# Kernel tuning notes

Measured on AMD Instinct MI355X. Metric: run time of the kernel, lower is better.

The kernel has to match this reference:

```python
import jax, jax.numpy as jnp
import numpy as np

CODEBOOK_DIM = 64
CODEBOOK_SLOTS = 512
TEMPERATURE = 0.5
BS, H, W = 16, 64, 64
EPS_G = 1e-10  # gumbel numerical floor
EPS_P = 1e-9   # matches probs.add(1e-09) in torch code


def setup_inputs() -> dict:
    key = jax.random.key(0)
    k1, k2, k3 = jax.random.split(key, 3)
    ze = jax.random.normal(k1, (BS, CODEBOOK_DIM, H, W), dtype=jnp.float32)
    codebook = jax.random.normal(k2, (CODEBOOK_SLOTS, CODEBOOK_DIM), dtype=jnp.float32)
    # uniform noise for Gumbel reparameterization of RelaxedOneHotCategorical.rsample
    u = jax.random.uniform(k3, (BS * H * W, CODEBOOK_SLOTS), dtype=jnp.float32)
    return {"ze": ze, "codebook": codebook, "u": u}


def reference(ze, codebook, u):
    bs, d, h, w = ze.shape
    K = codebook.shape[0]
    log_K = jnp.log(jnp.float32(K))
    # [bs, d, h, w] -> [N, d]
    ze_flat = jnp.transpose(ze, (0, 2, 3, 1)).reshape(-1, d)
    # squared euclidean distances via addmm: ||c||^2 + ||z||^2 - 2 z c^T  -> [N, K]
    distances = (
        jnp.sum(codebook * codebook, axis=1)[None, :]
        + jnp.sum(ze_flat * ze_flat, axis=1, keepdims=True)
        - 2.0 * (ze_flat @ codebook.T)
    )
    logits = -distances
    # Gumbel-softmax (relaxed one-hot categorical rsample)
    gumbel = -jnp.log(-jnp.log(u + EPS_G) + EPS_G)
    soft_onehot = jax.nn.softmax((logits + gumbel) / TEMPERATURE, axis=1)
    hard_indices = jnp.argmax(soft_onehot, axis=1).reshape(bs, h, w)
    # weighted codebook lookup: [N, K] @ [K, d] -> [bs, h, w, d] -> [bs, d, h, w]
    z_q = jnp.transpose((soft_onehot @ codebook).reshape(bs, h, w, d), (0, 3, 1, 2))
    probs = jax.nn.softmax(logits, axis=1)
    KL = jnp.mean(jnp.sum((probs * (jnp.log(probs + EPS_P) + log_K)).reshape(bs, -1), axis=1))
    commit_loss = jnp.mean(jnp.sum((probs * distances).reshape(bs, -1), axis=1))
    return (z_q, hard_indices, KL, commit_loss)
```

## Files before the change

kernel.cpp:

```cpp
#include <hip/hip_runtime.h>
#include <math.h>
#include <stdint.h>

#define IDX_OFF 4194304
#define KL_OFF  4259840
#define CM_OFF  4259841
#define LOG_K   6.238324625039508f

typedef _Float16 half8 __attribute__((ext_vector_type(8)));
typedef _Float16 half4 __attribute__((ext_vector_type(4)));
typedef float f32x4 __attribute__((ext_vector_type(4)));

__device__ __forceinline__ float sh16sum(float v){
#pragma unroll
  for (int m = 1; m < 16; m <<= 1) v += __shfl_xor(v, m, 64);
  return v;
}
__device__ __forceinline__ float sh16max(float v){
#pragma unroll
  for (int m = 1; m < 16; m <<= 1) v = fmaxf(v, __shfl_xor(v, m, 64));
  return v;
}

__global__ __launch_bounds__(64) void vq_pack(const float* __restrict__ cbk, void* __restrict__ ws){
  _Float16* W1H = (_Float16*)ws;
  _Float16* W1L = W1H + 32768;
  _Float16* W2H = W1L + 32768;
  float*    CCw = (float*)(W2H + 32768);
  const int slot = blockIdx.x, c = threadIdx.x;
  const float x = cbk[(slot << 6) + c];
  const _Float16 h = (_Float16)x;
  W1H[(slot << 6) + c] = h;
  W1L[(slot << 6) + c] = (_Float16)(x - (float)h);
  W2H[(c << 9) + slot] = h;
  float s = x * x;
#pragma unroll
  for (int m = 1; m < 64; m <<= 1) s += __shfl_xor(s, m, 64);
  if (c == 0) CCw[slot] = s;
}

struct SMem {
  _Float16 B1H[128*68];
  _Float16 B1L[128*68];
  _Float16 B2H[64*132];
  _Float16 ET[32*144];
  float ZT[32*66];
  float CC[512];
  float ZZ[32];
  float TM[128];
  float SM1[128], SM2[128], STt[128], AMv[128];
  int   AMi[128];
  float RED[16];
};

__global__ __launch_bounds__(512, 4) void vq_main(
    const float* __restrict__ ze, const float* __restrict__ uin,
    const void* __restrict__ ws, float* __restrict__ out)
{
  __shared__ SMem sm;
  const _Float16* W1H = (const _Float16*)ws;
  const _Float16* W1L = W1H + 32768;
  const _Float16* W2H = W1L + 32768;
  const float*    CCw = (const float*)(W2H + 32768);

  const int tid  = threadIdx.x;
  const int lane = tid & 63, l15 = lane & 15, quad = lane >> 4;
  const int wv   = tid >> 6, Mg = wv >> 2, Ng = wv & 3;
  const int blk  = blockIdx.x;
  const int bb   = blk >> 7, hh = (blk >> 1) & 63, w0 = (blk & 1) << 5;
  const int n0   = blk << 5;

  {
    const int c = tid >> 3, w4 = (tid & 7) << 2;
    const float4 v = *(const float4*)(ze + ((size_t)bb << 18) + (c << 12) + (hh << 6) + w0 + w4);
    sm.ZT[(w4+0)*66 + c] = v.x;
    sm.ZT[(w4+1)*66 + c] = v.y;
    sm.ZT[(w4+2)*66 + c] = v.z;
    sm.ZT[(w4+3)*66 + c] = v.w;
  }
  sm.CC[tid] = CCw[tid];
  __syncthreads();
  if (tid < 32){
    float s = 0.f;
#pragma unroll 8
    for (int c = 0; c < 64; ++c){ const float v = sm.ZT[tid*66 + c]; s = fmaf(v, v, s); }
    sm.ZZ[tid] = s;
  }
  __syncthreads();

  half8 zh[2], zl[2];
#pragma unroll
  for (int kc = 0; kc < 2; ++kc){
    const float* zp = &sm.ZT[(Mg*16 + l15)*66 + (kc<<5) + (quad<<3)];
#pragma unroll
    for (int j = 0; j < 8; ++j){
      const float x = zp[j];
      const _Float16 h = (_Float16)x;
      zh[kc][j] = h; zl[kc][j] = (_Float16)(x - (float)h);
    }
  }
  const int pos0 = Mg*16 + quad*4;
  float zzv[4];
#pragma unroll
  for (int r = 0; r < 4; ++r) zzv[r] = sm.ZZ[pos0 + r];

  float m1[4], s1[4], s2s[4], t1s[4], am[4]; int ki[4];
#pragma unroll
  for (int r = 0; r < 4; ++r){ m1[r]=-3.0e38f; s1[r]=0.f; s2s[r]=0.f; t1s[r]=0.f; am[r]=-3.0e38f; ki[r]=0; }
  f32x4 zacc = {0.f,0.f,0.f,0.f};

  const float* ub = uin + ((size_t)(n0 + pos0) << 9) + (Ng<<5) + l15;
  const int sl_s = tid >> 2, c16 = (tid & 3) << 4;
  const int c_s  = tid >> 3, sg  = (tid & 7) << 4;
  const uint4* s1hp = (const uint4*)(W1H + (sl_s << 6) + c16);
  const uint4* s1lp = (const uint4*)(W1L + (sl_s << 6) + c16);
  const uint4* s2hp = (const uint4*)(W2H + (c_s << 9) + sg);

#pragma unroll 1
  for (int st = 0; st < 4; ++st){
    float uval[2][4];
#pragma unroll
    for (int nt = 0; nt < 2; ++nt)
#pragma unroll
      for (int r = 0; r < 4; ++r)
        uval[nt][r] = ub[(st<<7) + (r<<9) + (nt<<4)];
    __syncthreads();
    {
      const uint4 a0 = s1hp[(st<<10)+0], a1 = s1hp[(st<<10)+1];
      const uint4 b0 = s1lp[(st<<10)+0], b1 = s1lp[(st<<10)+1];
      const uint4 c0 = s2hp[(st<<4)+0],  c1 = s2hp[(st<<4)+1];
      uint2* d1h = (uint2*)&sm.B1H[sl_s*68 + c16];
      uint2* d1l = (uint2*)&sm.B1L[sl_s*68 + c16];
      uint2* d2h = (uint2*)&sm.B2H[c_s*132 + sg];
      d1h[0] = make_uint2(a0.x,a0.y); d1h[1] = make_uint2(a0.z,a0.w);
      d1h[2] = make_uint2(a1.x,a1.y); d1h[3] = make_uint2(a1.z,a1.w);
      d1l[0] = make_uint2(b0.x,b0.y); d1l[1] = make_uint2(b0.z,b0.w);
      d1l[2] = make_uint2(b1.x,b1.y); d1l[3] = make_uint2(b1.z,b1.w);
      d2h[0] = make_uint2(c0.x,c0.y); d2h[1] = make_uint2(c0.z,c0.w);
      d2h[2] = make_uint2(c1.x,c1.y); d2h[3] = make_uint2(c1.z,c1.w);
    }
    __syncthreads();

    float lv[2][4], av[2][4], llv[2][4];
#pragma unroll
    for (int nt = 0; nt < 2; ++nt){
      f32x4 acc = {0.f,0.f,0.f,0.f};
      const int slotl = (Ng<<5) + (nt<<4) + l15;
#pragma unroll
      for (int kc = 0; kc < 2; ++kc){
        const _Float16* bp = &sm.B1H[slotl*68 + (kc<<5) + (quad<<3)];
        const _Float16* lp = &sm.B1L[slotl*68 + (kc<<5) + (quad<<3)];
        const half4 h0 = *(const half4*)bp, h1 = *(const half4*)(bp+4);
        const half4 g0 = *(const half4*)lp, g1 = *(const half4*)(lp+4);
        const half8 bh = __builtin_shufflevector(h0, h1, 0,1,2,3,4,5,6,7);
        const half8 bl = __builtin_shufflevector(g0, g1, 0,1,2,3,4,5,6,7);
        acc = __builtin_amdgcn_mfma_f32_16x16x32_f16(zh[kc], bh, acc, 0,0,0);
        acc = __builtin_amdgcn_mfma_f32_16x16x32_f16(zl[kc], bh, acc, 0,0,0);
        acc = __builtin_amdgcn_mfma_f32_16x16x32_f16(zh[kc], bl, acc, 0,0,0);
      }
      const float ccv = sm.CC[(st<<7) + slotl];
#pragma unroll
      for (int r = 0; r < 4; ++r){
        const float l = fmaf(2.f, acc[r], -ccv - zzv[r]);
        const float llu = -__logf(uval[nt][r] + 1e-10f) + 1e-10f;
        lv[nt][r] = l; llv[nt][r] = llu;
        av[nt][r] = l - __logf(llu);
      }
    }
#pragma unroll
    for (int r = 0; r < 4; ++r){
      const float ta = sh16max(fmaxf(av[0][r], av[1][r]));
      if (l15 == 0) sm.TM[(pos0 + r)*4 + Ng] = ta;
    }
    __syncthreads();
#pragma unroll
    for (int r = 0; r < 4; ++r){
      const int pos = pos0 + r;
      float M = m1[r];
#pragma unroll
      for (int g = 0; g < 4; ++g) M = fmaxf(M, sm.TM[pos*4 + g]);
      const float sc1h = __expf(m1[r] - M);
      const float sc1  = sc1h * sc1h;
      m1[r] = M;
      s1[r] *= sc1; zacc[r] *= sc1; s2s[r] *= sc1h; t1s[r] *= sc1h;
      const float t0  = __expf(av[0][r] - M);
      const float t1e = __expf(av[1][r] - M);
      const float e0 = t0*t0, e1 = t1e*t1e;
      s1[r] += e0 + e1;
      sm.ET[pos*144 + (Ng<<5) + l15]      = (_Float16)e0;
      sm.ET[pos*144 + (Ng<<5) + 16 + l15] = (_Float16)e1;
      const float p0 = t0*llv[0][r], p1 = t1e*llv[1][r];
      s2s[r] += p0 + p1;
      t1s[r] = fmaf(p0, lv[0][r], fmaf(p1, lv[1][r], t1s[r]));
      float bv; int bi;
      const int sbase = (st<<7) + (Ng<<5) + l15;
      if (av[0][r] >= av[1][r]) { bv = av[0][r]; bi = sbase; }
      else                      { bv = av[1][r]; bi = sbase + 16; }
      if (bv > am[r]){ am[r] = bv; ki[r] = bi; }
    }
    __syncthreads();
#pragma unroll
    for (int kc3 = 0; kc3 < 4; ++kc3){
      const half8 af = *(const half8*)&sm.ET[(Mg*16 + l15)*144 + (kc3<<5) + (quad<<3)];
      const _Float16* bp = &sm.B2H[(Ng*16 + l15)*132 + (kc3<<5) + (quad<<3)];
      const half4 h0 = *(const half4*)bp, h1 = *(const half4*)(bp + 4);
      const half8 bh = __builtin_shufflevector(h0, h1, 0,1,2,3,4,5,6,7);
      zacc = __builtin_amdgcn_mfma_f32_16x16x32_f16(af, bh, zacc, 0,0,0);
    }
  }

#pragma unroll
  for (int r = 0; r < 4; ++r){
    s1[r]  = sh16sum(s1[r]);
    s2s[r] = sh16sum(s2s[r]);
    t1s[r] = sh16sum(t1s[r]);
#pragma unroll
    for (int m = 1; m < 16; m <<= 1){
      const float vo = __shfl_xor(am[r], m, 64);
      const int   io = __shfl_xor(ki[r], m, 64);
      if (vo > am[r] || (vo == am[r] && io < ki[r])){ am[r] = vo; ki[r] = io; }
    }
    if (l15 == 0){
      const int pos = pos0 + r;
      sm.SM1[pos*4+Ng] = s1[r];
      sm.SM2[pos*4+Ng] = s2s[r];
      sm.STt[pos*4+Ng] = t1s[r];
      sm.AMv[pos*4+Ng] = am[r];
      sm.AMi[pos*4+Ng] = ki[r];
    }
  }
  __syncthreads();

  float kl = 0.f, cm = 0.f;
#pragma unroll
  for (int r = 0; r < 4; ++r){
    const int pos = pos0 + r;
    float s1t = 0.f, s2t = 0.f, t1t = 0.f;
#pragma unroll
    for (int g = 0; g < 4; ++g){ s1t += sm.SM1[pos*4+g]; s2t += sm.SM2[pos*4+g]; t1t += sm.STt[pos*4+g]; }
    zacc[r] *= (1.0f / s1t);
    if (Ng == 0){
      const float pl = t1t / s2t;
      kl += pl + LOG_K - m1[r] - __logf(s2t);
      cm -= pl;
      if (l15 == 0){
        float bv = -3.0e38f; int bi = 0;
#pragma unroll
        for (int g = 0; g < 4; ++g){
          const float v = sm.AMv[pos*4+g]; const int i = sm.AMi[pos*4+g];
          if (v > bv || (v == bv && i < bi)){ bv = v; bi = i; }
        }
        out[IDX_OFF + n0 + pos] = (float)bi;
      }
    }
  }
  {
    float k = (Ng==0 && l15==0) ? kl : 0.f;
    float c = (Ng==0 && l15==0) ? cm : 0.f;
#pragma unroll
    for (int m = 1; m < 64; m <<= 1){ k += __shfl_xor(k,m,64); c += __shfl_xor(c,m,64); }
    if (lane == 0){ sm.RED[wv] = k; sm.RED[wv+8] = c; }
  }
  float* ZB = sm.ZT;
#pragma unroll
  for (int r = 0; r < 4; ++r)
    ZB[(Ng*16 + l15)*33 + pos0 + r] = zacc[r];
  __syncthreads();
  if (tid == 0){
    float tk = 0.f, tc = 0.f;
#pragma unroll
    for (int i = 0; i < 8; ++i){ tk += sm.RED[i]; tc += sm.RED[i+8]; }
    atomicAdd(out + KL_OFF, tk * 0.0625f);
    atomicAdd(out + CM_OFF, tc * 0.0625f);
  }
#pragma unroll
  for (int it = 0; it < 4; ++it){
    const int flat = tid + (it << 9);
    const int c = flat >> 5, w = flat & 31;
    out[((size_t)bb << 18) + (c << 12) + (hh << 6) + w0 + w] = ZB[c*33 + w];
  }
}

extern "C" void kernel_launch(void* const* d_in, const int* in_sizes, int n_in,
                              void* d_out, int out_size, void* d_ws, size_t ws_size,
                              hipStream_t stream){
  const float* ze  = (const float*)d_in[0];
  const float* cbk = (const float*)d_in[1];
  const float* uin = (const float*)d_in[2];
  float* out = (float*)d_out;
  hipMemsetAsync(out + KL_OFF, 0, 2 * sizeof(float), stream);
  vq_pack<<<dim3(512), dim3(64), 0, stream>>>(cbk, d_ws);
  vq_main<<<dim3(2048), dim3(512), 0, stream>>>(ze, uin, d_ws, out);
}
```

Baseline: 292.9 us.

## Rewrite main kernel as per-wave 16-row tiles with register-resident codebook fragments

The main kernel now has each wave own 16 rows and loop over all 512 slots in groups of 16. The codebook is pre-packed in MFMA fragment layout in global memory and read straight into registers, so the shared-memory staging, the cross-wave max/sum exchanges and most barriers go away. The online softmax rescale is lazy: it only fires when the running max grows by more than a threshold, and the transposed MFMA layout keeps each row's state in one lane group. The trade-off is more global/L2 traffic for codebook fragments, since each wave rereads them, and more, smaller MFMAs per row.

```diff
diff --git a/kernel.cpp b/kernel.cpp
--- a/kernel.cpp
+++ b/kernel.cpp
@@ -6,278 +6,172 @@
 #define KL_OFF  4259840
 #define CM_OFF  4259841
 #define LOG_K   6.238324625039508f
+#define THR     2.0f
 
 typedef _Float16 half8 __attribute__((ext_vector_type(8)));
 typedef _Float16 half4 __attribute__((ext_vector_type(4)));
-typedef float f32x4 __attribute__((ext_vector_type(4)));
-
-__device__ __forceinline__ float sh16sum(float v){
-#pragma unroll
-  for (int m = 1; m < 16; m <<= 1) v += __shfl_xor(v, m, 64);
-  return v;
-}
-__device__ __forceinline__ float sh16max(float v){
-#pragma unroll
-  for (int m = 1; m < 16; m <<= 1) v = fmaxf(v, __shfl_xor(v, m, 64));
-  return v;
-}
+typedef float    f32x4 __attribute__((ext_vector_type(4)));
 
 __global__ __launch_bounds__(64) void vq_pack(const float* __restrict__ cbk, void* __restrict__ ws){
-  _Float16* W1H = (_Float16*)ws;
-  _Float16* W1L = W1H + 32768;
-  _Float16* W2H = W1L + 32768;
-  float*    CCw = (float*)(W2H + 32768);
+  _Float16* LAh = (_Float16*)ws;
+  _Float16* LAl = LAh + 32768;
+  _Float16* QAh = LAl + 32768;
+  float*    CCw = (float*)(QAh + 32768);
   const int slot = blockIdx.x, c = threadIdx.x;
   const float x = cbk[(slot << 6) + c];
   const _Float16 h = (_Float16)x;
-  W1H[(slot << 6) + c] = h;
-  W1L[(slot << 6) + c] = (_Float16)(x - (float)h);
-  W2H[(c << 9) + slot] = h;
+  const _Float16 l = (_Float16)(x - (float)h);
+  const int g = slot >> 4;
+  {
+    const int kc = c >> 5, quad = (c >> 3) & 3, j = c & 7;
+    const int lane = (quad << 4) | (slot & 15);
+    const int idx = ((((g << 1) | kc) << 6) | lane) * 8 + j;
+    LAh[idx] = h; LAl[idx] = l;
+  }
+  {
+    const int quad2 = (slot >> 2) & 3, j2 = slot & 3;
+    const int cg = c >> 4;
+    const int lane = (quad2 << 4) | (c & 15);
+    QAh[(((g << 6) | lane) << 4) | (cg << 2) | j2] = h;
+  }
   float s = x * x;
 #pragma unroll
   for (int m = 1; m < 64; m <<= 1) s += __shfl_xor(s, m, 64);
   if (c == 0) CCw[slot] = s;
 }
 
-struct SMem {
-  _Float16 B1H[128*68];
-  _Float16 B1L[128*68];
-  _Float16 B2H[64*132];
-  _Float16 ET[32*144];
-  float ZT[32*66];
-  float CC[512];
-  float ZZ[32];
-  float TM[128];
-  float SM1[128], SM2[128], STt[128], AMv[128];
-  int   AMi[128];
-  float RED[16];
-};
-
-__global__ __launch_bounds__(512, 4) void vq_main(
+__global__ __launch_bounds__(256, 4) void vq_main(
     const float* __restrict__ ze, const float* __restrict__ uin,
     const void* __restrict__ ws, float* __restrict__ out)
 {
-  __shared__ SMem sm;
-  const _Float16* W1H = (const _Float16*)ws;
-  const _Float16* W1L = W1H + 32768;
-  const _Float16* W2H = W1L + 32768;
-  const float*    CCw = (const float*)(W2H + 32768);
+  __shared__ float RED[8];
+  const _Float16* wsp = (const _Float16*)ws;
+  const half8* LAh = (const half8*)wsp;
+  const half8* LAl = (const half8*)(wsp + 32768);
+  const half4* QAh = (const half4*)(wsp + 65536);
+  const float* CCw = (const float*)(wsp + 98304);
 
   const int tid  = threadIdx.x;
   const int lane = tid & 63, l15 = lane & 15, quad = lane >> 4;
-  const int wv   = tid >> 6, Mg = wv >> 2, Ng = wv & 3;
-  const int blk  = blockIdx.x;
-  const int bb   = blk >> 7, hh = (blk >> 1) & 63, w0 = (blk & 1) << 5;
-  const int n0   = blk << 5;
+  const int wv   = tid >> 6;
+  const int n    = (blockIdx.x << 6) | (wv << 4) | l15;
+  const int bb   = n >> 12, hh = (n >> 6) & 63, w = n & 63;
 
-  {
-    const int c = tid >> 3, w4 = (tid & 7) << 2;
-    const float4 v = *(const float4*)(ze + ((size_t)bb << 18) + (c << 12) + (hh << 6) + w0 + w4);
-    sm.ZT[(w4+0)*66 + c] = v.x;
-    sm.ZT[(w4+1)*66 + c] = v.y;
-    sm.ZT[(w4+2)*66 + c] = v.z;
-    sm.ZT[(w4+3)*66 + c] = v.w;
-  }
-  sm.CC[tid] = CCw[tid];
-  __syncthreads();
-  if (tid < 32){
-    float s = 0.f;
-#pragma unroll 8
-    for (int c = 0; c < 64; ++c){ const float v = sm.ZT[tid*66 + c]; s = fmaf(v, v, s); }
-    sm.ZZ[tid] = s;
-  }
-  __syncthreads();
-
+  const float* zp = ze + ((size_t)bb << 18) + (hh << 6) + w;
   half8 zh[2], zl[2];
+  float zz = 0.f;
 #pragma unroll
-  for (int kc = 0; kc < 2; ++kc){
-    const float* zp = &sm.ZT[(Mg*16 + l15)*66 + (kc<<5) + (quad<<3)];
+  for (int kc = 0; kc < 2; ++kc)
 #pragma unroll
     for (int j = 0; j < 8; ++j){
-      const float x = zp[j];
+      const float x = zp[(size_t)((kc << 5) + (quad << 3) + j) << 12];
+      zz = fmaf(x, x, zz);
       const _Float16 h = (_Float16)x;
-      zh[kc][j] = h; zl[kc][j] = (_Float16)(x - (float)h);
+      zh[kc][j] = h;
+      zl[kc][j] = (_Float16)(x - (float)h);
     }
-  }
-  const int pos0 = Mg*16 + quad*4;
-  float zzv[4];
-#pragma unroll
-  for (int r = 0; r < 4; ++r) zzv[r] = sm.ZZ[pos0 + r];
+  zz += __shfl_xor(zz, 16, 64);
+  zz += __shfl_xor(zz, 32, 64);
 
-  float m1[4], s1[4], s2s[4], t1s[4], am[4]; int ki[4];
-#pragma unroll
-  for (int r = 0; r < 4; ++r){ m1[r]=-3.0e38f; s1[r]=0.f; s2s[r]=0.f; t1s[r]=0.f; am[r]=-3.0e38f; ki[r]=0; }
-  f32x4 zacc = {0.f,0.f,0.f,0.f};
+  float m1 = -3.0e38f, s1 = 0.f, s2s = 0.f, t1s = 0.f, am = -3.0e38f;
+  int   ki = 0;
+  f32x4 zq0 = {0.f,0.f,0.f,0.f}, zq1 = {0.f,0.f,0.f,0.f};
+  f32x4 zq2 = {0.f,0.f,0.f,0.f}, zq3 = {0.f,0.f,0.f,0.f};
 
-  const float* ub = uin + ((size_t)(n0 + pos0) << 9) + (Ng<<5) + l15;
-  const int sl_s = tid >> 2, c16 = (tid & 3) << 4;
-  const int c_s  = tid >> 3, sg  = (tid & 7) << 4;
-  const uint4* s1hp = (const uint4*)(W1H + (sl_s << 6) + c16);
-  const uint4* s1lp = (const uint4*)(W1L + (sl_s << 6) + c16);
-  const uint4* s2hp = (const uint4*)(W2H + (c_s << 9) + sg);
+  const float* uB = uin + ((size_t)n << 9) + (quad << 2);
 
-#pragma unroll 1
-  for (int st = 0; st < 4; ++st){
-    float uval[2][4];
-#pragma unroll
-    for (int nt = 0; nt < 2; ++nt)
-#pragma unroll
-      for (int r = 0; r < 4; ++r)
-        uval[nt][r] = ub[(st<<7) + (r<<9) + (nt<<4)];
-    __syncthreads();
-    {
-      const uint4 a0 = s1hp[(st<<10)+0], a1 = s1hp[(st<<10)+1];
-      const uint4 b0 = s1lp[(st<<10)+0], b1 = s1lp[(st<<10)+1];
-      const uint4 c0 = s2hp[(st<<4)+0],  c1 = s2hp[(st<<4)+1];
-      uint2* d1h = (uint2*)&sm.B1H[sl_s*68 + c16];
-      uint2* d1l = (uint2*)&sm.B1L[sl_s*68 + c16];
-      uint2* d2h = (uint2*)&sm.B2H[c_s*132 + sg];
-      d1h[0] = make_uint2(a0.x,a0.y); d1h[1] = make_uint2(a0.z,a0.w);
-      d1h[2] = make_uint2(a1.x,a1.y); d1h[3] = make_uint2(a1.z,a1.w);
-      d1l[0] = make_uint2(b0.x,b0.y); d1l[1] = make_uint2(b0.z,b0.w);
-      d1l[2] = make_uint2(b1.x,b1.y); d1l[3] = make_uint2(b1.z,b1.w);
-      d2h[0] = make_uint2(c0.x,c0.y); d2h[1] = make_uint2(c0.z,c0.w);
-      d2h[2] = make_uint2(c1.x,c1.y); d2h[3] = make_uint2(c1.z,c1.w);
-    }
-    __syncthreads();
+#pragma unroll 2
+  for (int g = 0; g < 32; ++g){
+    const float4 uf = *(const float4*)(uB + (g << 4));
+    const float4 c4 = *(const float4*)(CCw + (g << 4) + (quad << 2));
+    const half8 ch0 = LAh[((g << 1) | 0) * 64 + lane];
+    const half8 ch1 = LAh[((g << 1) | 1) * 64 + lane];
+    const half8 cl0 = LAl[((g << 1) | 0) * 64 + lane];
+    const half8 cl1 = LAl[((g << 1) | 1) * 64 + lane];
+    const int qb = ((g << 6) | lane) << 2;
+    const half4 qa0 = QAh[qb | 0], qa1 = QAh[qb | 1];
+    const half4 qa2 = QAh[qb | 2], qa3 = QAh[qb | 3];
 
-    float lv[2][4], av[2][4], llv[2][4];
-#pragma unroll
-    for (int nt = 0; nt < 2; ++nt){
-      f32x4 acc = {0.f,0.f,0.f,0.f};
-      const int slotl = (Ng<<5) + (nt<<4) + l15;
-#pragma unroll
-      for (int kc = 0; kc < 2; ++kc){
-        const _Float16* bp = &sm.B1H[slotl*68 + (kc<<5) + (quad<<3)];
-        const _Float16* lp = &sm.B1L[slotl*68 + (kc<<5) + (quad<<3)];
-        const half4 h0 = *(const half4*)bp, h1 = *(const half4*)(bp+4);
-        const half4 g0 = *(const half4*)lp, g1 = *(const half4*)(lp+4);
-        const half8 bh = __builtin_shufflevector(h0, h1, 0,1,2,3,4,5,6,7);
-        const half8 bl = __builtin_shufflevector(g0, g1, 0,1,2,3,4,5,6,7);
-        acc = __builtin_amdgcn_mfma_f32_16x16x32_f16(zh[kc], bh, acc, 0,0,0);
-        acc = __builtin_amdgcn_mfma_f32_16x16x32_f16(zl[kc], bh, acc, 0,0,0);
-        acc = __builtin_amdgcn_mfma_f32_16x16x32_f16(zh[kc], bl, acc, 0,0,0);
-      }
-      const float ccv = sm.CC[(st<<7) + slotl];
-#pragma unroll
-      for (int r = 0; r < 4; ++r){
-        const float l = fmaf(2.f, acc[r], -ccv - zzv[r]);
-        const float llu = -__logf(uval[nt][r] + 1e-10f) + 1e-10f;
-        lv[nt][r] = l; llv[nt][r] = llu;
-        av[nt][r] = l - __logf(llu);
-      }
-    }
+    f32x4 acc = {0.f,0.f,0.f,0.f};
+    acc = __builtin_amdgcn_mfma_f32_16x16x32_f16(ch0, zh[0], acc, 0,0,0);
+    acc = __builtin_amdgcn_mfma_f32_16x16x32_f16(cl0, zh[0], acc, 0,0,0);
+    acc = __builtin_amdgcn_mfma_f32_16x16x32_f16(ch0, zl[0], acc, 0,0,0);
+    acc = __builtin_amdgcn_mfma_f32_16x16x32_f16(ch1, zh[1], acc, 0,0,0);
+    acc = __builtin_amdgcn_mfma_f32_16x16x32_f16(cl1, zh[1], acc, 0,0,0);
+    acc = __builtin_amdgcn_mfma_f32_16x16x32_f16(ch1, zl[1], acc, 0,0,0);
+
+    const float ua[4] = {uf.x, uf.y, uf.z, uf.w};
+    const float ca[4] = {c4.x, c4.y, c4.z, c4.w};
+    float lg[4], lu[4], av[4];
 #pragma unroll
     for (int r = 0; r < 4; ++r){
-      const float ta = sh16max(fmaxf(av[0][r], av[1][r]));
-      if (l15 == 0) sm.TM[(pos0 + r)*4 + Ng] = ta;
+      lg[r] = fmaf(2.f, acc[r], -ca[r] - zz);
+      lu[r] = 1e-10f - __logf(ua[r] + 1e-10f);
+      av[r] = lg[r] - __logf(lu[r]);
     }
-    __syncthreads();
+    float pm = fmaxf(fmaxf(av[0], av[1]), fmaxf(av[2], av[3]));
+    pm = fmaxf(pm, __shfl_xor(pm, 16, 64));
+    pm = fmaxf(pm, __shfl_xor(pm, 32, 64));
+    if (pm > m1 + THR){
+      const float sc = __expf(m1 - pm), sc2 = sc * sc;
+      s1 *= sc2; s2s *= sc; t1s *= sc;
+      zq0 *= sc2; zq1 *= sc2; zq2 *= sc2; zq3 *= sc2;
+      m1 = pm;
+    }
+    half4 ef;
+    const int sb = (g << 4) | (quad << 2);
 #pragma unroll
     for (int r = 0; r < 4; ++r){
-      const int pos = pos0 + r;
-      float M = m1[r];
-#pragma unroll
-      for (int g = 0; g < 4; ++g) M = fmaxf(M, sm.TM[pos*4 + g]);
-      const float sc1h = __expf(m1[r] - M);
-      const float sc1  = sc1h * sc1h;
-      m1[r] = M;
-      s1[r] *= sc1; zacc[r] *= sc1; s2s[r] *= sc1h; t1s[r] *= sc1h;
-      const float t0  = __expf(av[0][r] - M);
-      const float t1e = __expf(av[1][r] - M);
-      const float e0 = t0*t0, e1 = t1e*t1e;
-      s1[r] += e0 + e1;
-      sm.ET[pos*144 + (Ng<<5) + l15]      = (_Float16)e0;
-      sm.ET[pos*144 + (Ng<<5) + 16 + l15] = (_Float16)e1;
-      const float p0 = t0*llv[0][r], p1 = t1e*llv[1][r];
-      s2s[r] += p0 + p1;
-      t1s[r] = fmaf(p0, lv[0][r], fmaf(p1, lv[1][r], t1s[r]));
-      float bv; int bi;
-      const int sbase = (st<<7) + (Ng<<5) + l15;
-      if (av[0][r] >= av[1][r]) { bv = av[0][r]; bi = sbase; }
-      else                      { bv = av[1][r]; bi = sbase + 16; }
-      if (bv > am[r]){ am[r] = bv; ki[r] = bi; }
+      const float t = __expf(av[r] - m1);
+      const float e = t * t;
+      s1 += e;
+      ef[r] = (_Float16)e;
+      const float p = t * lu[r];
+      s2s += p;
+      t1s = fmaf(p, lg[r], t1s);
+      if (av[r] > am){ am = av[r]; ki = sb + r; }
     }
-    __syncthreads();
-#pragma unroll
-    for (int kc3 = 0; kc3 < 4; ++kc3){
-      const half8 af = *(const half8*)&sm.ET[(Mg*16 + l15)*144 + (kc3<<5) + (quad<<3)];
-      const _Float16* bp = &sm.B2H[(Ng*16 + l15)*132 + (kc3<<5) + (quad<<3)];
-      const half4 h0 = *(const half4*)bp, h1 = *(const half4*)(bp + 4);
-      const half8 bh = __builtin_shufflevector(h0, h1, 0,1,2,3,4,5,6,7);
-      zacc = __builtin_amdgcn_mfma_f32_16x16x32_f16(af, bh, zacc, 0,0,0);
-    }
+    zq0 = __builtin_amdgcn_mfma_f32_16x16x16f16(qa0, ef, zq0, 0,0,0);
+    zq1 = __builtin_amdgcn_mfma_f32_16x16x16f16(qa1, ef, zq1, 0,0,0);
+    zq2 = __builtin_amdgcn_mfma_f32_16x16x16f16(qa2, ef, zq2, 0,0,0);
+    zq3 = __builtin_amdgcn_mfma_f32_16x16x16f16(qa3, ef, zq3, 0,0,0);
   }
 
 #pragma unroll
-  for (int r = 0; r < 4; ++r){
-    s1[r]  = sh16sum(s1[r]);
-    s2s[r] = sh16sum(s2s[r]);
-    t1s[r] = sh16sum(t1s[r]);
-#pragma unroll
-    for (int m = 1; m < 16; m <<= 1){
-      const float vo = __shfl_xor(am[r], m, 64);
-      const int   io = __shfl_xor(ki[r], m, 64);
-      if (vo > am[r] || (vo == am[r] && io < ki[r])){ am[r] = vo; ki[r] = io; }
-    }
-    if (l15 == 0){
-      const int pos = pos0 + r;
-      sm.SM1[pos*4+Ng] = s1[r];
-      sm.SM2[pos*4+Ng] = s2s[r];
-      sm.STt[pos*4+Ng] = t1s[r];
-      sm.AMv[pos*4+Ng] = am[r];
-      sm.AMi[pos*4+Ng] = ki[r];
-    }
+  for (int m = 16; m < 64; m <<= 1){
+    s1  += __shfl_xor(s1,  m, 64);
+    s2s += __shfl_xor(s2s, m, 64);
+    t1s += __shfl_xor(t1s, m, 64);
+    const float vo = __shfl_xor(am, m, 64);
+    const int   io = __shfl_xor(ki, m, 64);
+    if (vo > am || (vo == am && io < ki)){ am = vo; ki = io; }
   }
-  __syncthreads();
+  const float inv = 1.0f / s1;
+  const float pl  = t1s / s2s;
+  float kl = pl + LOG_K - m1 - __logf(s2s);
+  float cm = -pl;
+  if (quad == 0) out[IDX_OFF + n] = (float)ki;
 
-  float kl = 0.f, cm = 0.f;
+  float* ob = out + ((size_t)bb << 18) + (hh << 6) + w;
 #pragma unroll
   for (int r = 0; r < 4; ++r){
-    const int pos = pos0 + r;
-    float s1t = 0.f, s2t = 0.f, t1t = 0.f;
+    const int cb = (quad << 2) + r;
+    ob[(size_t)(cb     ) << 12] = zq0[r] * inv;
+    ob[(size_t)(cb + 16) << 12] = zq1[r] * inv;
+    ob[(size_t)(cb + 32) << 12] = zq2[r] * inv;
+    ob[(size_t)(cb + 48) << 12] = zq3[r] * inv;
+  }
+
+  if (quad != 0){ kl = 0.f; cm = 0.f; }
 #pragma unroll
-    for (int g = 0; g < 4; ++g){ s1t += sm.SM1[pos*4+g]; s2t += sm.SM2[pos*4+g]; t1t += sm.STt[pos*4+g]; }
-    zacc[r] *= (1.0f / s1t);
-    if (Ng == 0){
-      const float pl = t1t / s2t;
-      kl += pl + LOG_K - m1[r] - __logf(s2t);
-      cm -= pl;
-      if (l15 == 0){
-        float bv = -3.0e38f; int bi = 0;
+  for (int m = 1; m < 16; m <<= 1){ kl += __shfl_xor(kl, m, 64); cm += __shfl_xor(cm, m, 64); }
 #pragma unroll
-        for (int g = 0; g < 4; ++g){
-          const float v = sm.AMv[pos*4+g]; const int i = sm.AMi[pos*4+g];
-          if (v > bv || (v == bv && i < bi)){ bv = v; bi = i; }
-        }
-        out[IDX_OFF + n0 + pos] = (float)bi;
-      }
-    }
-  }
-  {
-    float k = (Ng==0 && l15==0) ? kl : 0.f;
-    float c = (Ng==0 && l15==0) ? cm : 0.f;
-#pragma unroll
-    for (int m = 1; m < 64; m <<= 1){ k += __shfl_xor(k,m,64); c += __shfl_xor(c,m,64); }
-    if (lane == 0){ sm.RED[wv] = k; sm.RED[wv+8] = c; }
-  }
-  float* ZB = sm.ZT;
-#pragma unroll
-  for (int r = 0; r < 4; ++r)
-    ZB[(Ng*16 + l15)*33 + pos0 + r] = zacc[r];
+  for (int m = 16; m < 64; m <<= 1){ kl += __shfl_xor(kl, m, 64); cm += __shfl_xor(cm, m, 64); }
+  if (lane == 0){ RED[wv] = kl; RED[wv + 4] = cm; }
   __syncthreads();
   if (tid == 0){
-    float tk = 0.f, tc = 0.f;
-#pragma unroll
-    for (int i = 0; i < 8; ++i){ tk += sm.RED[i]; tc += sm.RED[i+8]; }
-    atomicAdd(out + KL_OFF, tk * 0.0625f);
-    atomicAdd(out + CM_OFF, tc * 0.0625f);
-  }
-#pragma unroll
-  for (int it = 0; it < 4; ++it){
-    const int flat = tid + (it << 9);
-    const int c = flat >> 5, w = flat & 31;
-    out[((size_t)bb << 18) + (c << 12) + (hh << 6) + w0 + w] = ZB[c*33 + w];
+    atomicAdd(out + KL_OFF, (RED[0]+RED[1]+RED[2]+RED[3]) * 0.0625f);
+    atomicAdd(out + CM_OFF, (RED[4]+RED[5]+RED[6]+RED[7]) * 0.0625f);
   }
 }
 
@@ -290,5 +184,5 @@
   float* out = (float*)d_out;
   hipMemsetAsync(out + KL_OFF, 0, 2 * sizeof(float), stream);
   vq_pack<<<dim3(512), dim3(64), 0, stream>>>(cbk, d_ws);
-  vq_main<<<dim3(2048), dim3(512), 0, stream>>>(ze, uin, d_ws, out);
+  vq_main<<<dim3(1024), dim3(256), 0, stream>>>(ze, uin, d_ws, out);
 }
```

New measurement: 261.0 us. -10.9%, faster.
